# Optimization experiments

Measured on AMD Instinct MI355X. Metric: run time of the kernel, lower is better.

## Reference

```python
import jax, jax.numpy as jnp
import numpy as np

NB, CH, NY, NX, NC = 2, 64, 80, 80, 80
STRIDE = 4.0


def _conv(x, w, b, pad):
    y = jax.lax.conv_general_dilated(x, w, (1, 1), [(pad, pad), (pad, pad)],
                                     dimension_numbers=('NCHW', 'OIHW', 'NCHW'))
    return y + b[None, :, None, None]


def _head(x, w1, b1, w2, b2, final_relu):
    y = jax.nn.relu(_conv(x, w1, b1, 1))
    y = _conv(y, w2, b2, 0)
    return jax.nn.relu(y) if final_relu else y


def setup_inputs() -> dict:
    key = jax.random.key(0)
    ks = jax.random.split(key, 16)
    s = 0.05

    def cw(k, o, i, kk):
        return jax.random.normal(k, (o, i, kk, kk), jnp.float32) * s

    def cb(k, o):
        return jax.random.normal(k, (o,), jnp.float32) * s

    inp = {
        'x': jax.random.normal(ks[0], (NB, CH, NY, NX), jnp.float32),
        # offsets: [batch_index, off_x, off_y] per image (esod tile offsets)
        'offsets': jnp.concatenate([
            jnp.arange(NB, dtype=jnp.float32)[:, None],
            jax.random.uniform(ks[1], (NB, 2), jnp.float32) * 4.0], axis=1),
        'hm_w1': cw(ks[2], CH, CH, 3), 'hm_b1': cb(ks[3], CH),
        'hm_w2': cw(ks[4], NC, CH, 1), 'hm_b2': jnp.full((NC,), -2.19, jnp.float32),
        'wh_w1': cw(ks[5], CH, CH, 3), 'wh_b1': cb(ks[6], CH),
        'wh_w2': cw(ks[7], 2, CH, 1), 'wh_b2': cb(ks[8], 2),
        'reg_w1': cw(ks[9], CH, CH, 3), 'reg_b1': cb(ks[10], CH),
        'reg_w2': cw(ks[11], 2, CH, 1), 'reg_b2': cb(ks[12], 2),
    }
    return inp


def _forward(x, offsets, hm_w1, hm_b1, hm_w2, hm_b2,
             wh_w1, wh_b1, wh_w2, wh_b2,
             reg_w1, reg_b1, reg_w2, reg_b2):
    hm = _head(x, hm_w1, hm_b1, hm_w2, hm_b2, False)    # (nb, nc, ny, nx)
    wh = _head(x, wh_w1, wh_b1, wh_w2, wh_b2, True)     # (nb, 2, ny, nx)
    reg = _head(x, reg_w1, reg_b1, reg_w2, reg_b2, True)
    nb, nc, ny, nx = hm.shape

    wh_ = jnp.transpose(wh, (0, 2, 3, 1))   # (nb, ny, nx, 2)
    reg_ = jnp.transpose(reg, (0, 2, 3, 1))
    yv, xv = jnp.meshgrid(jnp.arange(ny), jnp.arange(nx), indexing='ij')
    grid = jnp.stack([xv, yv], -1).astype(jnp.float32)[None]  # (1, ny, nx, 2)

    off_xy = offsets[:, 1:3].reshape(nb, 1, 1, 2) * 2.0
    ctr = grid + off_xy + reg_
    bbox = jnp.concatenate([ctr - wh_ / 2.0, ctr + wh_ / 2.0], -1) * STRIDE  # xyxy

    # xyxy -> xywh (same per-image boxes for every class channel)
    cxy = (bbox[..., :2] + bbox[..., 2:]) / 2.0
    bwh = bbox[..., 2:] - bbox[..., :2]
    xywh = jnp.concatenate([cxy, bwh], -1)              # (nb, ny, nx, 4)

    hm_ = jax.nn.sigmoid(hm)
    hmax = jax.lax.reduce_window(hm_, -jnp.inf, jax.lax.max,
                                 (1, 1, 3, 3), (1, 1, 1, 1),
                                 [(0, 0), (0, 0), (1, 1), (1, 1)])
    maxima = (hmax == hm_)                              # (nb, nc, ny, nx)

    no = 5 + nc
    xywh_b = jnp.broadcast_to(xywh[:, None], (nb, nc, ny, nx, 4))
    score = hm_[..., None]
    oh = jnp.broadcast_to(jnp.eye(nc, dtype=hm_.dtype)[None, :, None, None, :],
                          (nb, nc, ny, nx, nc))
    rows = jnp.concatenate([xywh_b, score, oh], -1)     # (nb, nc, ny, nx, no)

    K = nc * ny * nx
    rows = rows.reshape(nb, K, no)
    m = maxima.reshape(nb, K)

    def compact(r, mk):
        # stable sort: maxima rows first, preserving (c, y, x) scan order
        order = jnp.argsort(jnp.logical_not(mk), stable=True)
        return r[order] * mk[order][:, None].astype(r.dtype)

    return jax.vmap(compact)(rows, m)                   # (nb, K, 5+nc), zero-padded


def reference(x, offsets, hm_w1, hm_b1, hm_w2, hm_b2,
              wh_w1, wh_b1, wh_w2, wh_b2,
              reg_w1, reg_b1, reg_w2, reg_b2):
    return _forward(x, offsets, hm_w1, hm_b1, hm_w2, hm_b2,
                    wh_w1, wh_b1, wh_w2, wh_b2,
                    reg_w1, reg_b1, reg_w2, reg_b2)
```

## Files before the change

### kernel.cpp

```cpp
#include <hip/hip_runtime.h>
#include <math.h>

#define NBATCH 2
#define CHN    64
#define NYY    80
#define NXX    80
#define NCLS   80
#define NPIX   6400
#define KTOT   512000
#define NOUT   85
#define NBLK   500

typedef float vf4 __attribute__((ext_vector_type(4)));

#define QTOT   21760000L
#define QF1    13056000L
#define QF2    13721600L
#define QF3    19584000L

__global__ __launch_bounds__(320)
void conv1_kernel(const float* __restrict__ x,
                  const float* __restrict__ hw1, const float* __restrict__ hb1,
                  const float* __restrict__ ww1, const float* __restrict__ wb1,
                  const float* __restrict__ rw1, const float* __restrict__ rb1,
                  double* __restrict__ c1hm, float* __restrict__ c1wr,
                  vf4* __restrict__ outq)
{
    __shared__ double smem_d[4992];
    const int bl = blockIdx.x;
    const int t  = threadIdx.x;

    const int gtid = bl * 320 + t;
    const int nth  = 640 * 320;
    const vf4 fz = {0.f, 0.f, 0.f, 0.f};

    if (bl < 320) {
        float*  lxf = (float*)smem_d;
        double* lwd = (double*)((char*)smem_d + 21504);

        const int yt  = bl % 40;
        const int ocg = (bl / 40) % 4;
        const int b   = bl / 160;

        const int pxq = t % 80;
        const int ocq = t / 80;
        const int r   = pxq / 40;
        const int c   = (pxq % 40) * 2;
        const int oc0 = ocg * 16 + ocq * 4;
        const int gy0 = yt * 2;

        const float* xin = x + (size_t)b * CHN * NPIX;

        double acc[2][4];
        #pragma unroll
        for (int j = 0; j < 2; j++)
            #pragma unroll
            for (int o = 0; o < 4; o++) acc[j][o] = (double)hb1[oc0 + o];

        for (int cc = 0; cc < 4; cc++) {
            const int icc = cc * 16;
            __syncthreads();
            for (int j = t; j < 1280; j += 320) {
                int ic_l = j / 80; int rem = j % 80;
                int row_l = rem / 20; int c4 = (rem % 20) * 4;
                int gy = gy0 - 1 + row_l;
                float4 v = make_float4(0.f, 0.f, 0.f, 0.f);
                if ((unsigned)gy < 80u)
                    v = *(const float4*)(xin + (size_t)(icc + ic_l) * NPIX + gy * NXX + c4);
                float* dst = &lxf[(ic_l * 4 + row_l) * 84];
                dst[c4 + 1] = v.x; dst[c4 + 2] = v.y;
                dst[c4 + 3] = v.z; dst[c4 + 4] = v.w;
            }
            for (int j = t; j < 64; j += 320) {
                lxf[j * 84 + 0]  = 0.f;
                lxf[j * 84 + 81] = 0.f;
            }
            for (int j = t; j < 2304; j += 320) {
                int oc_l = j % 16; int k = j / 16;
                int ic_l = k / 9, tap = k % 9;
                lwd[k * 16 + oc_l] =
                    (double)hw1[((size_t)(ocg * 16 + oc_l) * CHN + icc + ic_l) * 9 + tap];
            }
            __syncthreads();
            {
                int i0 = cc * 16, i1 = i0 + 16;
                for (int i = i0; i < i1; i++) {
                    long q = (long)gtid + (long)i * nth;
                    if (q < QF1) __builtin_nontemporal_store(fz, outq + q);
                }
            }
            for (int ic = 0; ic < 16; ic++) {
                double xw[3][4];
                #pragma unroll
                for (int ky = 0; ky < 3; ky++) {
                    const float* row = &lxf[(ic * 4 + r + ky) * 84];
                    float2 a  = *(const float2*)&row[c];
                    float2 bb = *(const float2*)&row[c + 2];
                    xw[ky][0] = (double)a.x;  xw[ky][1] = (double)a.y;
                    xw[ky][2] = (double)bb.x; xw[ky][3] = (double)bb.y;
                }
                #pragma unroll
                for (int ky = 0; ky < 3; ky++)
                #pragma unroll
                for (int kx = 0; kx < 3; kx++) {
                    const double* wv = &lwd[(ic * 9 + ky * 3 + kx) * 16 + ocq * 4];
                    double w0 = wv[0], w1d = wv[1], w2 = wv[2], w3 = wv[3];
                    double x0 = xw[ky][kx], x1 = xw[ky][kx + 1];
                    acc[0][0] += x0 * w0; acc[0][1] += x0 * w1d;
                    acc[0][2] += x0 * w2; acc[0][3] += x0 * w3;
                    acc[1][0] += x1 * w0; acc[1][1] += x1 * w1d;
                    acc[1][2] += x1 * w2; acc[1][3] += x1 * w3;
                }
            }
        }
        size_t pix = (size_t)(gy0 + r) * NXX + c;
        #pragma unroll
        for (int o = 0; o < 4; o++) {
            double2 v;
            v.x = acc[0][o] > 0.0 ? acc[0][o] : 0.0;
            v.y = acc[1][o] > 0.0 ? acc[1][o] : 0.0;
            *(double2*)(c1hm + ((size_t)b * CHN + oc0 + o) * NPIX + pix) = v;
        }
    } else {
        float* lxw = (float*)smem_d;
        float* lwf = (float*)((char*)smem_d + 30720);

        const int blw = bl - 320;
        const int yt  = blw % 20;
        const int ocg = (blw / 20) % 4;
        const int img = blw / 80;

        const int head = img >> 1, b = img & 1;
        const float* w1 = (head == 0) ? ww1 : rw1;
        const float* b1 = (head == 0) ? wb1 : rb1;
        const float* xin = x + (size_t)b * CHN * NPIX;

        const int pxq = t % 80;
        const int ocq = t / 80;
        const int r   = pxq / 20;
        const int c   = (pxq % 20) * 4;
        const int oc0 = ocg * 16 + ocq * 4;
        const int gy0 = yt * 4;

        float acc[4][4];
        #pragma unroll
        for (int j = 0; j < 4; j++)
            #pragma unroll
            for (int o = 0; o < 4; o++) acc[j][o] = b1[oc0 + o];

        for (int cc = 0; cc < 4; cc++) {
            const int icc = cc * 16;
            __syncthreads();
            for (int j = t; j < 1920; j += 320) {
                int ic_l = j / 120; int rem = j % 120;
                int row_l = rem / 20; int c4 = (rem % 20) * 4;
                int gy = gy0 - 1 + row_l;
                float4 v = make_float4(0.f, 0.f, 0.f, 0.f);
                if ((unsigned)gy < 80u)
                    v = *(const float4*)(xin + (size_t)(icc + ic_l) * NPIX + gy * NXX + c4);
                *(float4*)&lxw[(ic_l * 6 + row_l) * 80 + c4] = v;
            }
            for (int j = t; j < 2304; j += 320) {
                int oc_l = j % 16; int k = j / 16;
                int ic_l = k / 9, tap = k % 9;
                lwf[k * 16 + oc_l] =
                    w1[((size_t)(ocg * 16 + oc_l) * CHN + icc + ic_l) * 9 + tap];
            }
            __syncthreads();
            {
                int i0 = cc * 16, i1 = i0 + 16;
                for (int i = i0; i < i1; i++) {
                    long q = (long)gtid + (long)i * nth;
                    if (q < QF1) __builtin_nontemporal_store(fz, outq + q);
                }
            }
            for (int ic = 0; ic < 16; ic++) {
                float xw[3][6];
                #pragma unroll
                for (int ky = 0; ky < 3; ky++) {
                    const float* row = &lxw[(ic * 6 + r + ky) * 80];
                    xw[ky][0] = (c > 0) ? row[c - 1] : 0.f;
                    float4 m = *(const float4*)&row[c];
                    xw[ky][1] = m.x; xw[ky][2] = m.y;
                    xw[ky][3] = m.z; xw[ky][4] = m.w;
                    xw[ky][5] = (c < 76) ? row[c + 4] : 0.f;
                }
                #pragma unroll
                for (int ky = 0; ky < 3; ky++)
                #pragma unroll
                for (int kx = 0; kx < 3; kx++) {
                    const float* wv = &lwf[(ic * 9 + ky * 3 + kx) * 16 + ocq * 4];
                    float w0 = wv[0], w1v = wv[1], w2 = wv[2], w3 = wv[3];
                    #pragma unroll
                    for (int j = 0; j < 4; j++) {
                        float xv = xw[ky][j + kx];
                        acc[j][0] += xv * w0; acc[j][1] += xv * w1v;
                        acc[j][2] += xv * w2; acc[j][3] += xv * w3;
                    }
                }
            }
        }
        size_t pix = (size_t)(gy0 + r) * NXX + c;
        #pragma unroll
        for (int o = 0; o < 4; o++) {
            float4 v;
            v.x = fmaxf(acc[0][o], 0.f); v.y = fmaxf(acc[1][o], 0.f);
            v.z = fmaxf(acc[2][o], 0.f); v.w = fmaxf(acc[3][o], 0.f);
            *(float4*)(c1wr + ((size_t)img * CHN + oc0 + o) * NPIX + pix) = v;
        }
    }
}

__global__ __launch_bounds__(256)
void conv2_hm_kernel(const double* __restrict__ c1,
                     const float* __restrict__ w2,
                     const float* __restrict__ b2,
                     double* __restrict__ hm_z,
                     vf4* __restrict__ outq)
{
    __shared__ double lx[64 * 64];
    __shared__ double lw[64 * 80];

    const int bl  = blockIdx.x;
    const int t   = threadIdx.x;
    const int b   = bl / 100;
    const int px0 = (bl % 100) * 64;

    {
        const int gtid = bl * 256 + t;
        const vf4 fz = {0.f, 0.f, 0.f, 0.f};
        for (int i = 0; i < 13; i++) {
            long q = QF1 + (long)gtid + (long)i * 51200;
            if (q < QF2) __builtin_nontemporal_store(fz, outq + q);
        }
    }

    const double* in = c1 + (size_t)b * CHN * NPIX;
    for (int j = t; j < 4096; j += 256) {
        int ic = j >> 6, px = j & 63;
        lx[j] = in[(size_t)ic * NPIX + px0 + px];
    }
    for (int j = t; j < 5120; j += 256) {
        int ic = j / 80, oc = j % 80;
        lw[j] = (double)w2[(size_t)oc * CHN + ic];
    }
    __syncthreads();

    const int px  = t & 63;
    const int ocg = t >> 6;
    double acc[20];
    #pragma unroll
    for (int o = 0; o < 20; o++) acc[o] = (double)b2[ocg * 20 + o];

    for (int ic = 0; ic < 64; ic++) {
        double xv = lx[ic * 64 + px];
        const double* wrow = &lw[ic * 80 + ocg * 20];
        #pragma unroll
        for (int o = 0; o < 20; o++) acc[o] += xv * wrow[o];
    }
    #pragma unroll
    for (int o = 0; o < 20; o++)
        hm_z[((size_t)b * NCLS + ocg * 20 + o) * NPIX + px0 + px] = acc[o];
}

__global__ __launch_bounds__(256)
void conv2_wr_kernel(const float* __restrict__ c1,
                     const float* __restrict__ wh_w2, const float* __restrict__ wh_b2,
                     const float* __restrict__ rg_w2, const float* __restrict__ rg_b2,
                     float* __restrict__ wh, float* __restrict__ rg)
{
    int p  = blockIdx.x * 256 + threadIdx.x;
    int hc = blockIdx.y;
    int b  = blockIdx.z;
    int head = hc >> 1, ch = hc & 1;

    const float* in = c1 + ((size_t)(head * 2 + b) * CHN) * NPIX;
    const float* w  = (head == 0) ? wh_w2 + (size_t)ch * CHN : rg_w2 + (size_t)ch * CHN;
    float bias      = (head == 0) ? wh_b2[ch] : rg_b2[ch];

    float acc = bias;
    for (int ic = 0; ic < CHN; ic++) acc += in[(size_t)ic * NPIX + p] * w[ic];
    acc = fmaxf(acc, 0.f);
    float* o = (head == 0) ? wh : rg;
    o[((size_t)b * 2 + ch) * NPIX + p] = acc;
}

__global__ void flags_kernel(const double* __restrict__ hm_z,
                             unsigned long long* __restrict__ ballots,
                             unsigned int* __restrict__ counts,
                             vf4* __restrict__ outq)
{
    int b = blockIdx.y;
    int k = blockIdx.x * 1024 + threadIdx.x;

    {
        const int gtid = (b * NBLK + blockIdx.x) * 1024 + threadIdx.x;
        const vf4 fz = {0.f, 0.f, 0.f, 0.f};
        for (int i = 0; i < 6; i++) {
            long q = QF2 + (long)gtid + (long)i * 1024000;
            if (q < QF3) __builtin_nontemporal_store(fz, outq + q);
        }
    }

    int c = k / NPIX;
    int p = k - c * NPIX;
    int y = p / NXX, xx = p - y * NXX;

    const double* h = hm_z + ((size_t)b * NCLS + c) * NPIX;
    double s = h[p];
    double m = s;
    #pragma unroll
    for (int dy = -1; dy <= 1; dy++) {
        int yy = y + dy;
        if ((unsigned)yy >= (unsigned)NYY) continue;
        const double* hr = h + yy * NXX;
        #pragma unroll
        for (int dx = -1; dx <= 1; dx++) {
            int xn = xx + dx;
            if ((unsigned)xn >= (unsigned)NXX) continue;
            double v = hr[xn];
            m = v > m ? v : m;
        }
    }
    bool flag = (s == m);
    unsigned long long ball = __ballot(flag);
    int lane = threadIdx.x & 63;
    int wave = threadIdx.x >> 6;

    __shared__ unsigned int wcnt[16];
    if (lane == 0) {
        ballots[(size_t)b * 8000 + blockIdx.x * 16 + wave] = ball;
        wcnt[wave] = __popcll(ball);
    }
    __syncthreads();
    if (threadIdx.x == 0) {
        unsigned int tot = 0;
        for (int i = 0; i < 16; i++) tot += wcnt[i];
        counts[b * NBLK + blockIdx.x] = tot;
    }
}

__global__ void scan_kernel(const unsigned int* __restrict__ counts,
                            unsigned int* __restrict__ offs)
{
    int b = blockIdx.x;
    int t = threadIdx.x;
    unsigned int v = (t < NBLK) ? counts[b * NBLK + t] : 0u;
    unsigned int xi = v;
    #pragma unroll
    for (int d = 1; d < 64; d <<= 1) {
        unsigned int n = __shfl_up(xi, d, 64);
        if ((t & 63) >= d) xi += n;
    }
    __shared__ unsigned int wtot[8];
    __shared__ unsigned int wbase[8];
    if ((t & 63) == 63) wtot[t >> 6] = xi;
    __syncthreads();
    if (t == 0) {
        unsigned int a = 0;
        for (int i = 0; i < 8; i++) { wbase[i] = a; a += wtot[i]; }
    }
    __syncthreads();
    unsigned int excl = xi - v + wbase[t >> 6];
    if (t < NBLK) offs[b * NBLK + t] = excl;
}

__global__ void scatter_kernel(const unsigned long long* __restrict__ ballots,
                               const unsigned int* __restrict__ offs,
                               const double* __restrict__ hm_z,
                               const float* __restrict__ wh,
                               const float* __restrict__ rg,
                               const float* __restrict__ offsets,
                               float* __restrict__ out,
                               vf4* __restrict__ outq)
{
    int b = blockIdx.y;
    int k = blockIdx.x * 1024 + threadIdx.x;
    int lane = threadIdx.x & 63;
    int wave = threadIdx.x >> 6;

    {
        const int gtid = (b * NBLK + blockIdx.x) * 1024 + threadIdx.x;
        const vf4 fz = {0.f, 0.f, 0.f, 0.f};
        for (int i = 0; i < 3; i++) {
            long q = QF3 + (long)gtid + (long)i * 1024000;
            if (q < QTOT) __builtin_nontemporal_store(fz, outq + q);
        }
    }

    unsigned long long ball = ballots[(size_t)b * 8000 + blockIdx.x * 16 + wave];

    __shared__ unsigned int wc[16];
    __shared__ unsigned int wb[16];
    if (lane == 0) wc[wave] = __popcll(ball);
    __syncthreads();
    if (threadIdx.x == 0) {
        unsigned int a = 0;
        for (int i = 0; i < 16; i++) { wb[i] = a; a += wc[i]; }
    }
    __syncthreads();

    bool flag = (ball >> lane) & 1ull;
    if (!flag) return;

    unsigned int rank = offs[b * NBLK + blockIdx.x] + wb[wave]
                      + (unsigned int)__popcll(ball & ((1ull << lane) - 1ull));

    int c = k / NPIX;
    int p = k - c * NPIX;
    int y = p / NXX, xx = p - y * NXX;

    float offx = offsets[b * 3 + 1];
    float offy = offsets[b * 3 + 2];
    float r0 = rg[((size_t)b * 2 + 0) * NPIX + p];
    float r1 = rg[((size_t)b * 2 + 1) * NPIX + p];
    float w0 = wh[((size_t)b * 2 + 0) * NPIX + p];
    float w1 = wh[((size_t)b * 2 + 1) * NPIX + p];
    double z = hm_z[((size_t)b * NCLS + c) * NPIX + p];
    float s  = (float)(1.0 / (1.0 + exp(-z)));

    float cx = ((float)xx + 2.f * offx + r0) * 4.f;
    float cy = ((float)y  + 2.f * offy + r1) * 4.f;

    float* row = out + ((size_t)b * KTOT + rank) * NOUT;
    row[0] = cx;
    row[1] = cy;
    row[2] = w0 * 4.f;
    row[3] = w1 * 4.f;
    row[4] = s;
    row[5 + c] = 1.f;
}

extern "C" void kernel_launch(void* const* d_in, const int* in_sizes, int n_in,
                              void* d_out, int out_size, void* d_ws, size_t ws_size,
                              hipStream_t stream)
{
    const float* x       = (const float*)d_in[0];
    const float* offsets = (const float*)d_in[1];
    const float* hm_w1   = (const float*)d_in[2];
    const float* hm_b1   = (const float*)d_in[3];
    const float* hm_w2   = (const float*)d_in[4];
    const float* hm_b2   = (const float*)d_in[5];
    const float* wh_w1   = (const float*)d_in[6];
    const float* wh_b1   = (const float*)d_in[7];
    const float* wh_w2   = (const float*)d_in[8];
    const float* wh_b2   = (const float*)d_in[9];
    const float* reg_w1  = (const float*)d_in[10];
    const float* reg_b1  = (const float*)d_in[11];
    const float* reg_w2  = (const float*)d_in[12];
    const float* reg_b2  = (const float*)d_in[13];

    float* out = (float*)d_out;
    vf4* outq  = (vf4*)d_out;

    char* wp = (char*)d_ws;
    double* c1hm = (double*)wp;                 wp += (size_t)NBATCH * CHN * NPIX * 8;
    double* hm_z = (double*)wp;                 wp += (size_t)NBATCH * NCLS * NPIX * 8;
    float*  c1wr = (float*)wp;                  wp += (size_t)2 * NBATCH * CHN * NPIX * 4;
    float*  wh   = (float*)wp;                  wp += (size_t)NBATCH * 2 * NPIX * 4;
    float*  rg   = (float*)wp;                  wp += (size_t)NBATCH * 2 * NPIX * 4;
    unsigned long long* ballots = (unsigned long long*)wp; wp += (size_t)NBATCH * 8000 * 8;
    unsigned int* counts = (unsigned int*)wp;   wp += (size_t)NBATCH * NBLK * 4;
    unsigned int* offs   = (unsigned int*)wp;

    conv1_kernel<<<640, 320, 0, stream>>>(
        x, hm_w1, hm_b1, wh_w1, wh_b1, reg_w1, reg_b1, c1hm, c1wr, outq);

    conv2_hm_kernel<<<200, 256, 0, stream>>>(c1hm, hm_w2, hm_b2, hm_z, outq);

    conv2_wr_kernel<<<dim3(25, 4, 2), 256, 0, stream>>>(
        c1wr, wh_w2, wh_b2, reg_w2, reg_b2, wh, rg);

    flags_kernel<<<dim3(NBLK, 2), 1024, 0, stream>>>(hm_z, ballots, counts, outq);

    scan_kernel<<<2, 512, 0, stream>>>(counts, offs);

    scatter_kernel<<<dim3(NBLK, 2), 1024, 0, stream>>>(
        ballots, offs, hm_z, wh, rg, offsets, out, outq);
}
```

Before: 158.6 us.

## Retile fp64 heatmap conv, interleave head blocks, merge conv2 kernels

The fp64 heatmap branch of the first 3x3 conv now computes 4 pixels per thread over 4-row tiles, up from 2 pixels over 2-row tiles. This halves its block count and reuses each loaded weight across more pixels. Heatmap blocks are interleaved every third block with the fp32 wh/reg blocks to balance load, for a 480-block grid. The two 1x1 conv kernels are merged into a single launch, and the output-zeroing ranges are rebalanced across the kernels. The trade-offs are more fp64 registers per thread for the heatmap path and a larger shared-memory footprint.

```diff
diff --git a/kernel.cpp b/kernel.cpp
--- a/kernel.cpp
+++ b/kernel.cpp
@@ -14,9 +14,9 @@
 typedef float vf4 __attribute__((ext_vector_type(4)));
 
 #define QTOT   21760000L
-#define QF1    13056000L
-#define QF2    13721600L
-#define QF3    19584000L
+#define QF1    11980800L
+#define QF2    15257600L
+#define QF3    20377600L
 
 __global__ __launch_bounds__(320)
 void conv1_kernel(const float* __restrict__ x,
@@ -26,127 +26,38 @@
                   double* __restrict__ c1hm, float* __restrict__ c1wr,
                   vf4* __restrict__ outq)
 {
-    __shared__ double smem_d[4992];
+    __shared__ double smem_d[6144];
     const int bl = blockIdx.x;
     const int t  = threadIdx.x;
 
     const int gtid = bl * 320 + t;
-    const int nth  = 640 * 320;
+    const int nth  = 480 * 320;
     const vf4 fz = {0.f, 0.f, 0.f, 0.f};
 
-    if (bl < 320) {
-        float*  lxf = (float*)smem_d;
-        double* lwd = (double*)((char*)smem_d + 21504);
-
-        const int yt  = bl % 40;
-        const int ocg = (bl / 40) % 4;
-        const int b   = bl / 160;
-
-        const int pxq = t % 80;
-        const int ocq = t / 80;
-        const int r   = pxq / 40;
-        const int c   = (pxq % 40) * 2;
+    const int pxq = t % 80;
+    const int ocq = t / 80;
+    const int r   = pxq / 20;
+    const int c   = (pxq % 20) * 4;
+
+    float* lxf = (float*)smem_d;
+
+    if (bl % 3 == 0) {
+        double* lwd = (double*)((char*)smem_d + 30720);
+
+        const int idx = bl / 3;
+        const int yt  = idx % 20;
+        const int ocg = (idx / 20) % 4;
+        const int b   = idx / 80;
         const int oc0 = ocg * 16 + ocq * 4;
-        const int gy0 = yt * 2;
+        const int gy0 = yt * 4;
 
         const float* xin = x + (size_t)b * CHN * NPIX;
 
-        double acc[2][4];
-        #pragma unroll
-        for (int j = 0; j < 2; j++)
+        double acc[4][4];
+        #pragma unroll
+        for (int j = 0; j < 4; j++)
             #pragma unroll
             for (int o = 0; o < 4; o++) acc[j][o] = (double)hb1[oc0 + o];
-
-        for (int cc = 0; cc < 4; cc++) {
-            const int icc = cc * 16;
-            __syncthreads();
-            for (int j = t; j < 1280; j += 320) {
-                int ic_l = j / 80; int rem = j % 80;
-                int row_l = rem / 20; int c4 = (rem % 20) * 4;
-                int gy = gy0 - 1 + row_l;
-                float4 v = make_float4(0.f, 0.f, 0.f, 0.f);
-                if ((unsigned)gy < 80u)
-                    v = *(const float4*)(xin + (size_t)(icc + ic_l) * NPIX + gy * NXX + c4);
-                float* dst = &lxf[(ic_l * 4 + row_l) * 84];
-                dst[c4 + 1] = v.x; dst[c4 + 2] = v.y;
-                dst[c4 + 3] = v.z; dst[c4 + 4] = v.w;
-            }
-            for (int j = t; j < 64; j += 320) {
-                lxf[j * 84 + 0]  = 0.f;
-                lxf[j * 84 + 81] = 0.f;
-            }
-            for (int j = t; j < 2304; j += 320) {
-                int oc_l = j % 16; int k = j / 16;
-                int ic_l = k / 9, tap = k % 9;
-                lwd[k * 16 + oc_l] =
-                    (double)hw1[((size_t)(ocg * 16 + oc_l) * CHN + icc + ic_l) * 9 + tap];
-            }
-            __syncthreads();
-            {
-                int i0 = cc * 16, i1 = i0 + 16;
-                for (int i = i0; i < i1; i++) {
-                    long q = (long)gtid + (long)i * nth;
-                    if (q < QF1) __builtin_nontemporal_store(fz, outq + q);
-                }
-            }
-            for (int ic = 0; ic < 16; ic++) {
-                double xw[3][4];
-                #pragma unroll
-                for (int ky = 0; ky < 3; ky++) {
-                    const float* row = &lxf[(ic * 4 + r + ky) * 84];
-                    float2 a  = *(const float2*)&row[c];
-                    float2 bb = *(const float2*)&row[c + 2];
-                    xw[ky][0] = (double)a.x;  xw[ky][1] = (double)a.y;
-                    xw[ky][2] = (double)bb.x; xw[ky][3] = (double)bb.y;
-                }
-                #pragma unroll
-                for (int ky = 0; ky < 3; ky++)
-                #pragma unroll
-                for (int kx = 0; kx < 3; kx++) {
-                    const double* wv = &lwd[(ic * 9 + ky * 3 + kx) * 16 + ocq * 4];
-                    double w0 = wv[0], w1d = wv[1], w2 = wv[2], w3 = wv[3];
-                    double x0 = xw[ky][kx], x1 = xw[ky][kx + 1];
-                    acc[0][0] += x0 * w0; acc[0][1] += x0 * w1d;
-                    acc[0][2] += x0 * w2; acc[0][3] += x0 * w3;
-                    acc[1][0] += x1 * w0; acc[1][1] += x1 * w1d;
-                    acc[1][2] += x1 * w2; acc[1][3] += x1 * w3;
-                }
-            }
-        }
-        size_t pix = (size_t)(gy0 + r) * NXX + c;
-        #pragma unroll
-        for (int o = 0; o < 4; o++) {
-            double2 v;
-            v.x = acc[0][o] > 0.0 ? acc[0][o] : 0.0;
-            v.y = acc[1][o] > 0.0 ? acc[1][o] : 0.0;
-            *(double2*)(c1hm + ((size_t)b * CHN + oc0 + o) * NPIX + pix) = v;
-        }
-    } else {
-        float* lxw = (float*)smem_d;
-        float* lwf = (float*)((char*)smem_d + 30720);
-
-        const int blw = bl - 320;
-        const int yt  = blw % 20;
-        const int ocg = (blw / 20) % 4;
-        const int img = blw / 80;
-
-        const int head = img >> 1, b = img & 1;
-        const float* w1 = (head == 0) ? ww1 : rw1;
-        const float* b1 = (head == 0) ? wb1 : rb1;
-        const float* xin = x + (size_t)b * CHN * NPIX;
-
-        const int pxq = t % 80;
-        const int ocq = t / 80;
-        const int r   = pxq / 20;
-        const int c   = (pxq % 20) * 4;
-        const int oc0 = ocg * 16 + ocq * 4;
-        const int gy0 = yt * 4;
-
-        float acc[4][4];
-        #pragma unroll
-        for (int j = 0; j < 4; j++)
-            #pragma unroll
-            for (int o = 0; o < 4; o++) acc[j][o] = b1[oc0 + o];
 
         for (int cc = 0; cc < 4; cc++) {
             const int icc = cc * 16;
@@ -158,7 +69,93 @@
                 float4 v = make_float4(0.f, 0.f, 0.f, 0.f);
                 if ((unsigned)gy < 80u)
                     v = *(const float4*)(xin + (size_t)(icc + ic_l) * NPIX + gy * NXX + c4);
-                *(float4*)&lxw[(ic_l * 6 + row_l) * 80 + c4] = v;
+                *(float4*)&lxf[(ic_l * 6 + row_l) * 80 + c4] = v;
+            }
+            for (int j = t; j < 2304; j += 320) {
+                int oc_l = j % 16; int k = j / 16;
+                int ic_l = k / 9, tap = k % 9;
+                lwd[k * 16 + oc_l] =
+                    (double)hw1[((size_t)(ocg * 16 + oc_l) * CHN + icc + ic_l) * 9 + tap];
+            }
+            __syncthreads();
+            {
+                int i0 = cc * 20, i1 = (cc == 3) ? 78 : cc * 20 + 20;
+                for (int i = i0; i < i1; i++) {
+                    long q = (long)gtid + (long)i * nth;
+                    if (q < QF1) __builtin_nontemporal_store(fz, outq + q);
+                }
+            }
+            for (int ic = 0; ic < 16; ic++) {
+                double xw[3][6];
+                #pragma unroll
+                for (int ky = 0; ky < 3; ky++) {
+                    const float* row = &lxf[(ic * 6 + r + ky) * 80];
+                    xw[ky][0] = (c > 0) ? (double)row[c - 1] : 0.0;
+                    float4 m = *(const float4*)&row[c];
+                    xw[ky][1] = (double)m.x; xw[ky][2] = (double)m.y;
+                    xw[ky][3] = (double)m.z; xw[ky][4] = (double)m.w;
+                    xw[ky][5] = (c < 76) ? (double)row[c + 4] : 0.0;
+                }
+                #pragma unroll
+                for (int ky = 0; ky < 3; ky++)
+                #pragma unroll
+                for (int kx = 0; kx < 3; kx++) {
+                    const double* wv = &lwd[(ic * 9 + ky * 3 + kx) * 16 + ocq * 4];
+                    double w0 = wv[0], w1d = wv[1], w2 = wv[2], w3 = wv[3];
+                    #pragma unroll
+                    for (int j = 0; j < 4; j++) {
+                        double xv = xw[ky][j + kx];
+                        acc[j][0] += xv * w0; acc[j][1] += xv * w1d;
+                        acc[j][2] += xv * w2; acc[j][3] += xv * w3;
+                    }
+                }
+            }
+        }
+        size_t pix = (size_t)(gy0 + r) * NXX + c;
+        #pragma unroll
+        for (int o = 0; o < 4; o++) {
+            double* dst = c1hm + ((size_t)b * CHN + oc0 + o) * NPIX + pix;
+            double2 lo, hi;
+            lo.x = acc[0][o] > 0.0 ? acc[0][o] : 0.0;
+            lo.y = acc[1][o] > 0.0 ? acc[1][o] : 0.0;
+            hi.x = acc[2][o] > 0.0 ? acc[2][o] : 0.0;
+            hi.y = acc[3][o] > 0.0 ? acc[3][o] : 0.0;
+            *(double2*)dst = lo;
+            *(double2*)(dst + 2) = hi;
+        }
+    } else {
+        float* lwf = (float*)((char*)smem_d + 30720);
+
+        const int idx = bl - bl / 3 - 1;
+        const int yt  = idx % 20;
+        const int ocg = (idx / 20) % 4;
+        const int img = idx / 80;
+
+        const int head = img >> 1, b = img & 1;
+        const float* w1 = (head == 0) ? ww1 : rw1;
+        const float* b1 = (head == 0) ? wb1 : rb1;
+        const float* xin = x + (size_t)b * CHN * NPIX;
+
+        const int oc0 = ocg * 16 + ocq * 4;
+        const int gy0 = yt * 4;
+
+        float acc[4][4];
+        #pragma unroll
+        for (int j = 0; j < 4; j++)
+            #pragma unroll
+            for (int o = 0; o < 4; o++) acc[j][o] = b1[oc0 + o];
+
+        for (int cc = 0; cc < 4; cc++) {
+            const int icc = cc * 16;
+            __syncthreads();
+            for (int j = t; j < 1920; j += 320) {
+                int ic_l = j / 120; int rem = j % 120;
+                int row_l = rem / 20; int c4 = (rem % 20) * 4;
+                int gy = gy0 - 1 + row_l;
+                float4 v = make_float4(0.f, 0.f, 0.f, 0.f);
+                if ((unsigned)gy < 80u)
+                    v = *(const float4*)(xin + (size_t)(icc + ic_l) * NPIX + gy * NXX + c4);
+                *(float4*)&lxf[(ic_l * 6 + row_l) * 80 + c4] = v;
             }
             for (int j = t; j < 2304; j += 320) {
                 int oc_l = j % 16; int k = j / 16;
@@ -168,7 +165,7 @@
             }
             __syncthreads();
             {
-                int i0 = cc * 16, i1 = i0 + 16;
+                int i0 = cc * 20, i1 = (cc == 3) ? 78 : cc * 20 + 20;
                 for (int i = i0; i < i1; i++) {
                     long q = (long)gtid + (long)i * nth;
                     if (q < QF1) __builtin_nontemporal_store(fz, outq + q);
@@ -178,7 +175,7 @@
                 float xw[3][6];
                 #pragma unroll
                 for (int ky = 0; ky < 3; ky++) {
-                    const float* row = &lxw[(ic * 6 + r + ky) * 80];
+                    const float* row = &lxf[(ic * 6 + r + ky) * 80];
                     xw[ky][0] = (c > 0) ? row[c - 1] : 0.f;
                     float4 m = *(const float4*)&row[c];
                     xw[ky][1] = m.x; xw[ky][2] = m.y;
@@ -212,77 +209,76 @@
 }
 
 __global__ __launch_bounds__(256)
-void conv2_hm_kernel(const double* __restrict__ c1,
-                     const float* __restrict__ w2,
-                     const float* __restrict__ b2,
-                     double* __restrict__ hm_z,
-                     vf4* __restrict__ outq)
-{
-    __shared__ double lx[64 * 64];
-    __shared__ double lw[64 * 80];
-
-    const int bl  = blockIdx.x;
-    const int t   = threadIdx.x;
-    const int b   = bl / 100;
-    const int px0 = (bl % 100) * 64;
+void conv2_kernel(const double* __restrict__ c1hm,
+                  const float* __restrict__ hm_w2, const float* __restrict__ hm_b2,
+                  const float* __restrict__ c1wr,
+                  const float* __restrict__ wh_w2, const float* __restrict__ wh_b2,
+                  const float* __restrict__ rg_w2, const float* __restrict__ rg_b2,
+                  double* __restrict__ hm_z, float* __restrict__ wh, float* __restrict__ rg,
+                  vf4* __restrict__ outq)
+{
+    __shared__ double smem2[9216];
+    const int bl = blockIdx.x;
+    const int t  = threadIdx.x;
 
     {
         const int gtid = bl * 256 + t;
         const vf4 fz = {0.f, 0.f, 0.f, 0.f};
-        for (int i = 0; i < 13; i++) {
-            long q = QF1 + (long)gtid + (long)i * 51200;
+        for (int i = 0; i < 32; i++) {
+            long q = QF1 + (long)gtid + (long)i * 102400;
             if (q < QF2) __builtin_nontemporal_store(fz, outq + q);
         }
     }
 
-    const double* in = c1 + (size_t)b * CHN * NPIX;
-    for (int j = t; j < 4096; j += 256) {
-        int ic = j >> 6, px = j & 63;
-        lx[j] = in[(size_t)ic * NPIX + px0 + px];
-    }
-    for (int j = t; j < 5120; j += 256) {
-        int ic = j / 80, oc = j % 80;
-        lw[j] = (double)w2[(size_t)oc * CHN + ic];
-    }
-    __syncthreads();
-
-    const int px  = t & 63;
-    const int ocg = t >> 6;
-    double acc[20];
-    #pragma unroll
-    for (int o = 0; o < 20; o++) acc[o] = (double)b2[ocg * 20 + o];
-
-    for (int ic = 0; ic < 64; ic++) {
-        double xv = lx[ic * 64 + px];
-        const double* wrow = &lw[ic * 80 + ocg * 20];
-        #pragma unroll
-        for (int o = 0; o < 20; o++) acc[o] += xv * wrow[o];
-    }
-    #pragma unroll
-    for (int o = 0; o < 20; o++)
-        hm_z[((size_t)b * NCLS + ocg * 20 + o) * NPIX + px0 + px] = acc[o];
-}
-
-__global__ __launch_bounds__(256)
-void conv2_wr_kernel(const float* __restrict__ c1,
-                     const float* __restrict__ wh_w2, const float* __restrict__ wh_b2,
-                     const float* __restrict__ rg_w2, const float* __restrict__ rg_b2,
-                     float* __restrict__ wh, float* __restrict__ rg)
-{
-    int p  = blockIdx.x * 256 + threadIdx.x;
-    int hc = blockIdx.y;
-    int b  = blockIdx.z;
-    int head = hc >> 1, ch = hc & 1;
-
-    const float* in = c1 + ((size_t)(head * 2 + b) * CHN) * NPIX;
-    const float* w  = (head == 0) ? wh_w2 + (size_t)ch * CHN : rg_w2 + (size_t)ch * CHN;
-    float bias      = (head == 0) ? wh_b2[ch] : rg_b2[ch];
-
-    float acc = bias;
-    for (int ic = 0; ic < CHN; ic++) acc += in[(size_t)ic * NPIX + p] * w[ic];
-    acc = fmaxf(acc, 0.f);
-    float* o = (head == 0) ? wh : rg;
-    o[((size_t)b * 2 + ch) * NPIX + p] = acc;
+    if (bl < 200) {
+        double* lx = smem2;
+        double* lw = smem2 + 4096;
+
+        const int b   = bl / 100;
+        const int px0 = (bl % 100) * 64;
+
+        const double* in = c1hm + (size_t)b * CHN * NPIX;
+        for (int j = t; j < 4096; j += 256) {
+            int ic = j >> 6, px = j & 63;
+            lx[j] = in[(size_t)ic * NPIX + px0 + px];
+        }
+        for (int j = t; j < 5120; j += 256) {
+            int ic = j / 80, oc = j % 80;
+            lw[j] = (double)hm_w2[(size_t)oc * CHN + ic];
+        }
+        __syncthreads();
+
+        const int px  = t & 63;
+        const int ocg = t >> 6;
+        double acc[20];
+        #pragma unroll
+        for (int o = 0; o < 20; o++) acc[o] = (double)hm_b2[ocg * 20 + o];
+
+        for (int ic = 0; ic < 64; ic++) {
+            double xv = lx[ic * 64 + px];
+            const double* wrow = &lw[ic * 80 + ocg * 20];
+            #pragma unroll
+            for (int o = 0; o < 20; o++) acc[o] += xv * wrow[o];
+        }
+        #pragma unroll
+        for (int o = 0; o < 20; o++)
+            hm_z[((size_t)b * NCLS + ocg * 20 + o) * NPIX + px0 + px] = acc[o];
+    } else {
+        const int blw  = bl - 200;
+        const int chunk = blw % 25;
+        const int hc   = (blw / 25) % 4;
+        const int b    = blw / 100;
+        const int head = hc >> 1, ch = hc & 1;
+
+        const int p = chunk * 256 + t;
+        const float* in = c1wr + ((size_t)(head * 2 + b) * CHN) * NPIX;
+        const float* w  = (head == 0) ? wh_w2 + (size_t)ch * CHN : rg_w2 + (size_t)ch * CHN;
+        float acc = (head == 0) ? wh_b2[ch] : rg_b2[ch];
+        for (int ic = 0; ic < CHN; ic++) acc += in[(size_t)ic * NPIX + p] * w[ic];
+        acc = fmaxf(acc, 0.f);
+        float* o = (head == 0) ? wh : rg;
+        o[((size_t)b * 2 + ch) * NPIX + p] = acc;
+    }
 }
 
 __global__ void flags_kernel(const double* __restrict__ hm_z,
@@ -296,7 +292,7 @@
     {
         const int gtid = (b * NBLK + blockIdx.x) * 1024 + threadIdx.x;
         const vf4 fz = {0.f, 0.f, 0.f, 0.f};
-        for (int i = 0; i < 6; i++) {
+        for (int i = 0; i < 5; i++) {
             long q = QF2 + (long)gtid + (long)i * 1024000;
             if (q < QF3) __builtin_nontemporal_store(fz, outq + q);
         }
@@ -382,7 +378,7 @@
     {
         const int gtid = (b * NBLK + blockIdx.x) * 1024 + threadIdx.x;
         const vf4 fz = {0.f, 0.f, 0.f, 0.f};
-        for (int i = 0; i < 3; i++) {
+        for (int i = 0; i < 2; i++) {
             long q = QF3 + (long)gtid + (long)i * 1024000;
             if (q < QTOT) __builtin_nontemporal_store(fz, outq + q);
         }
@@ -463,13 +459,12 @@
     unsigned int* counts = (unsigned int*)wp;   wp += (size_t)NBATCH * NBLK * 4;
     unsigned int* offs   = (unsigned int*)wp;
 
-    conv1_kernel<<<640, 320, 0, stream>>>(
+    conv1_kernel<<<480, 320, 0, stream>>>(
         x, hm_w1, hm_b1, wh_w1, wh_b1, reg_w1, reg_b1, c1hm, c1wr, outq);
 
-    conv2_hm_kernel<<<200, 256, 0, stream>>>(c1hm, hm_w2, hm_b2, hm_z, outq);
-
-    conv2_wr_kernel<<<dim3(25, 4, 2), 256, 0, stream>>>(
-        c1wr, wh_w2, wh_b2, reg_w2, reg_b2, wh, rg);
+    conv2_kernel<<<400, 256, 0, stream>>>(
+        c1hm, hm_w2, hm_b2, c1wr, wh_w2, wh_b2, reg_w2, reg_b2,
+        hm_z, wh, rg, outq);
 
     flags_kernel<<<dim3(NBLK, 2), 1024, 0, stream>>>(hm_z, ballots, counts, outq);
 
```

Measured after the change: 151.8 us. -4.3%, faster.
